# Kernel tuning notes

Measured on AMD Instinct MI355X. Metric: run time of the kernel, lower is better.

The kernel has to match this reference:

```python
import jax, jax.numpy as jnp
import numpy as np


def setup_inputs() -> dict:
    key = jax.random.key(0)
    k1, k2 = jax.random.split(key)
    B, N, M, D = 8, 2048, 2048, 1024
    x = jax.random.normal(k1, (B, N, D), dtype=jnp.float32)
    y = jax.random.normal(k2, (B, M, D), dtype=jnp.float32)
    return {"x": x, "y": y}


def reference(x, y):
    # scores: [B, N, M] = x @ y^T
    scores = jnp.einsum("bnd,bmd->bnm", x, y)
    # row-normalized attention over M (axis=2 of scores)
    attn_row = jax.nn.softmax(scores, axis=2)
    # column-normalized attention: softmax over N of scores^T, i.e. axis=1 then transpose
    attn_col = jax.nn.softmax(scores, axis=1)  # [B, N, M], normalized over N
    A = jnp.einsum("bnm,bmd->bnd", attn_row, y)          # attended summary of y per x-token
    Bout = jnp.einsum("bnm,bnd->bmd", attn_col, x)       # attended summary of x per y-token
    return (A, Bout)
```

## Files before the change

### kernel.cpp

```cpp
#include <hip/hip_runtime.h>
#include <cstdint>
#include <cstddef>

namespace {

constexpr int Bb = 8;
constexpr int Nn = 2048;
constexpr int Dd = 1024;
constexpr int NT = 64;

typedef _Float16 half8 __attribute__((ext_vector_type(8)));
typedef float f32x4v __attribute__((ext_vector_type(4)));
typedef float f32x16v __attribute__((ext_vector_type(16)));
typedef unsigned int v2u __attribute__((ext_vector_type(2)));
typedef unsigned int v4u __attribute__((ext_vector_type(4)));

__device__ __forceinline__ float fast_exp2(float x) {
  float r;
  asm("v_exp_f32 %0, %1\n\ts_nop 1" : "=v"(r) : "v"(x));
  return r;
}

__device__ __forceinline__ unsigned cvt2(float a, float b) {
  return __builtin_bit_cast(unsigned, __builtin_amdgcn_cvt_pkrtz(a, b));
}

__device__ __forceinline__ void barrier_lgkm() {
  asm volatile("s_waitcnt lgkmcnt(0)" ::: "memory");
  __builtin_amdgcn_s_barrier();
  __builtin_amdgcn_sched_barrier(0);
}
__device__ __forceinline__ void barrier_plain() {
  __builtin_amdgcn_s_barrier();
  __builtin_amdgcn_sched_barrier(0);
}

__global__ void convf16(const float* __restrict__ in, v4u* __restrict__ out) {
  const int n8 = Bb * Nn * Dd / 8;
  int i = blockIdx.x * blockDim.x + threadIdx.x;
  const int stride = gridDim.x * blockDim.x;
  const f32x4v* in4 = (const f32x4v*)in;
  for (; i < n8; i += stride) {
    f32x4v a = in4[2 * i], b = in4[2 * i + 1];
    v4u p;
    p[0] = cvt2(a[0], a[1]);
    p[1] = cvt2(a[2], a[3]);
    p[2] = cvt2(b[0], b[1]);
    p[3] = cvt2(b[2], b[3]);
    out[i] = p;
  }
}

template <int WS>
__device__ __forceinline__ v4u ld8h(const float* f32p, const v4u* h16p) {
  if constexpr (WS) {
    return *h16p;
  } else {
    f32x4v a = *(const f32x4v*)f32p;
    f32x4v b = *(const f32x4v*)(f32p + 4);
    v4u p;
    p[0] = cvt2(a[0], a[1]);
    p[1] = cvt2(a[2], a[3]);
    p[2] = cvt2(b[0], b[1]);
    p[3] = cvt2(b[2], b[3]);
    return p;
  }
}

template <int WS>
__global__ __launch_bounds__(512, 2) void flash_fwd(
    const float* __restrict__ Qf, const float* __restrict__ Yf,
    const v4u* __restrict__ Qw, const v4u* __restrict__ Yw,
    float* __restrict__ Om) {
  __shared__ __attribute__((aligned(128))) char ybuf[65536];
  __shared__ __attribute__((aligned(16))) char pscr[16384];
  __shared__ __attribute__((aligned(16))) char Pb[2048];
  __shared__ float sscale[32];
  __shared__ float sinvl[32];
  __shared__ int sflag[2];

  const int tid = (int)threadIdx.x;
  const int w = tid >> 6, l = tid & 63;
  const int lm = l & 15, g = (l >> 4) & 3, g2 = (l >> 5) & 1, l31 = l & 31;
  const int kvf = w >> 2, ds = w & 3;
  const int bid = (int)blockIdx.x, batch = bid & 7, row0 = (bid >> 3) * 32;
  const size_t bY = (size_t)batch * Nn;

  v4u qreg[2][8];
#pragma unroll
  for (int qh = 0; qh < 2; ++qh)
#pragma unroll
    for (int ks = 0; ks < 8; ++ks) {
      const int rr = row0 + qh * 16 + lm;
      const int dd_ = ds * 256 + ks * 32 + g * 8;
      qreg[qh][ks] = ld8h<WS>(Qf + (size_t)(bY + rr) * Dd + dd_,
                              Qw + (size_t)(bY + rr) * 128 + (dd_ >> 3));
    }

#define LOADY(dst, t_)                                                        \
  do {                                                                        \
    const int rr_ = (t_)*32 + kvf * 16 + lm;                                  \
    _Pragma("unroll") for (int ks = 0; ks < 8; ++ks) {                        \
      const int dd_ = ds * 256 + ks * 32 + g * 8;                             \
      dst[ks] = ld8h<WS>(Yf + (size_t)(bY + rr_) * Dd + dd_,                  \
                         Yw + (size_t)(bY + rr_) * 128 + (dd_ >> 3));         \
    }                                                                         \
  } while (0)

  const unsigned sbase =
      (unsigned)((kvf * 4 + (lm >> 2)) * 8192 + (ds * 16 + (g >> 1)) * 128 +
                 (lm & 3) * 32 + (g & 1) * 16);
#define STAGE_WR(SRC)                                                         \
  do {                                                                        \
    _Pragma("unroll") for (int ks = 0; ks < 8; ++ks)                          \
        *(v4u*)(ybuf + sbase + ks * 256) = SRC[ks];                           \
  } while (0)

  v4u sA[8], sB[8];
  LOADY(sA, 0);
  STAGE_WR(sA);

  f32x16v Oacc[4];
#pragma unroll
  for (int i = 0; i < 4; ++i)
#pragma unroll
    for (int j = 0; j < 16; ++j) Oacc[i][j] = 0.0f;

  float m_run = -__builtin_inff();
  float l_run = 0.0f;
  const unsigned ylds = (unsigned)(uintptr_t)&ybuf[0];
  constexpr float L2E = 1.44269504088896f;

  __syncthreads();

#define TILE_BODY(CUR, NXT, t_)                                               \
  do {                                                                        \
    f32x4v acc0 = {0.f, 0.f, 0.f, 0.f}, acc1 = {0.f, 0.f, 0.f, 0.f};          \
    _Pragma("unroll") for (int ks = 0; ks < 8; ++ks) {                        \
      half8 av = __builtin_bit_cast(half8, CUR[ks]);                          \
      acc0 = __builtin_amdgcn_mfma_f32_16x16x32_f16(                          \
          av, __builtin_bit_cast(half8, qreg[0][ks]), acc0, 0, 0, 0);         \
      acc1 = __builtin_amdgcn_mfma_f32_16x16x32_f16(                          \
          av, __builtin_bit_cast(half8, qreg[1][ks]), acc1, 0, 0, 0);         \
    }                                                                         \
    LOADY(NXT, ((t_) + 1) & 63);                                              \
    *(f32x4v*)(pscr + (w * 2 + 0) * 1024 + l * 16) = acc0;                    \
    *(f32x4v*)(pscr + (w * 2 + 1) * 1024 + l * 16) = acc1;                    \
    barrier_lgkm();                       \
    if (w < 2) {                                                              \
      const int qh = w;                                                       \
      f32x4v sa = {0.f, 0.f, 0.f, 0.f}, sb = {0.f, 0.f, 0.f, 0.f};            \
      _Pragma("unroll") for (int s = 0; s < 4; ++s) {                         \
        sa += *(const f32x4v*)(pscr + (s * 2 + qh) * 1024 + l * 16);          \
        sb += *(const f32x4v*)(pscr + ((s + 4) * 2 + qh) * 1024 + l * 16);    \
      }                                                                       \
      float pm = fmaxf(fmaxf(fmaxf(sa[0], sa[1]), fmaxf(sa[2], sa[3])),       \
                       fmaxf(fmaxf(sb[0], sb[1]), fmaxf(sb[2], sb[3])));      \
      pm = fmaxf(pm, __shfl_xor(pm, 16));                                     \
      pm = fmaxf(pm, __shfl_xor(pm, 32));                                     \
      bool defer = (pm <= m_run + 8.0f);                                      \
      bool allw = (bool)__all((int)defer);                                    \
      float scale = 1.0f;                                                     \
      if (!allw) {                                                            \
        float mn = fmaxf(m_run, pm);                                          \
        scale = fast_exp2((m_run - mn) * L2E);                                \
        m_run = mn;                                                           \
      }                                                                       \
      f32x4v ea, eb;                                                          \
      _Pragma("unroll") for (int i = 0; i < 4; ++i) {                         \
        ea[i] = fast_exp2((sa[i] - m_run) * L2E);                             \
        eb[i] = fast_exp2((sb[i] - m_run) * L2E);                             \
      }                                                                       \
      float ps = (ea[0] + ea[1]) + (ea[2] + ea[3]) + (eb[0] + eb[1]) +        \
                 (eb[2] + eb[3]);                                             \
      ps += __shfl_xor(ps, 16);                                               \
      ps += __shfl_xor(ps, 32);                                               \
      l_run = l_run * scale + ps;                                             \
      const int q_ = qh * 16 + lm;                                            \
      v2u pw0, pw1;                                                           \
      pw0[0] = cvt2(ea[0], ea[1]);                                            \
      pw0[1] = cvt2(ea[2], ea[3]);                                            \
      pw1[0] = cvt2(eb[0], eb[1]);                                            \
      pw1[1] = cvt2(eb[2], eb[3]);                                            \
      *(v2u*)(Pb + (g >> 1) * 512 + q_ * 16 + (g & 1) * 8) = pw0;             \
      *(v2u*)(Pb + (2 + (g >> 1)) * 512 + q_ * 16 + (g & 1) * 8) = pw1;       \
      if (l < 16) sscale[q_] = scale;                                         \
      if (l == 0) sflag[qh] = allw ? 0 : 1;                                   \
    }                                                                         \
    barrier_lgkm();                                \
    if (sflag[0] | sflag[1]) {                                                \
      _Pragma("unroll") for (int df = 0; df < 4; ++df)                        \
          _Pragma("unroll") for (int r = 0; r < 16; ++r) {                    \
        const int q_ = (r & 3) + 8 * (r >> 2) + 4 * g2;                       \
        Oacc[df][r] *= sscale[q_];                                            \
      }                                                                       \
    }                                                                         \
    _Pragma("unroll") for (int kb = 0; kb < 2; ++kb) {                        \
      half8 pa = *(const half8*)(Pb + (kb * 2 + g2) * 512 + l31 * 16);        \
      v2u trr[8];                                                             \
      _Pragma("unroll") for (int df = 0; df < 4; ++df) {                      \
        const unsigned wb =                                                   \
            ylds + (unsigned)((kb * 4 + g2 * 2) * 8192 +                      \
                              ((w * 4 + df) * 2 + (l31 >> 4)) * 128 +         \
                              (l31 & 15) * 8);                                \
        asm volatile("ds_read_b64_tr_b16 %0, %1"                              \
                     : "=v"(trr[df * 2])                                      \
                     : "v"(wb));                                              \
        asm volatile("ds_read_b64_tr_b16 %0, %1"                              \
                     : "=v"(trr[df * 2 + 1])                                  \
                     : "v"(wb + 8192u));                                      \
      }                                                                       \
    asm volatile("s_waitcnt lgkmcnt(0)" ::: "memory");                        \
    __builtin_amdgcn_sched_barrier(0);                                        \
      _Pragma("unroll") for (int df = 0; df < 4; ++df) {                      \
        v4u bu;                                                               \
        bu[0] = trr[df * 2][0];                                               \
        bu[1] = trr[df * 2][1];                                               \
        bu[2] = trr[df * 2 + 1][0];                                           \
        bu[3] = trr[df * 2 + 1][1];                                           \
        Oacc[df] = __builtin_amdgcn_mfma_f32_32x32x16_f16(                    \
            pa, __builtin_bit_cast(half8, bu), Oacc[df], 0, 0, 0);            \
      }                                                                       \
    }                                                                         \
    barrier_plain();                        \
    STAGE_WR(NXT);                                                            \
  } while (0)

  for (int t = 0; t < NT; t += 2) {
    TILE_BODY(sA, sB, t);
    TILE_BODY(sB, sA, t + 1);
  }

  if (w < 2 && l < 16) sinvl[w * 16 + lm] = 1.0f / l_run;
  __syncthreads();
#pragma unroll
  for (int df = 0; df < 4; ++df)
#pragma unroll
    for (int r = 0; r < 16; ++r) {
      const int q_ = (r & 3) + 8 * (r >> 2) + 4 * g2;
      const float inv = sinvl[q_];
      Om[(size_t)(bY + row0 + q_) * Dd + (w * 4 + df) * 32 + l31] =
          Oacc[df][r] * inv;
    }
#undef TILE_BODY
#undef STAGE_WR
#undef LOADY
}

}

extern "C" void kernel_launch(void* const* d_in, const int* in_sizes, int n_in,
                              void* d_out, int out_size, void* d_ws,
                              size_t ws_size, hipStream_t stream) {
  (void)in_sizes; (void)n_in; (void)out_size;
  const float* x = (const float*)d_in[0];
  const float* y = (const float*)d_in[1];
  float* A = (float*)d_out;
  float* Bo = A + (size_t)Bb * Nn * Dd;
  const size_t halfws = (size_t)Bb * Nn * Dd * 2;
  dim3 fg(512), fb(512);
  if (d_ws != nullptr && ws_size >= 2 * halfws) {
    v4u* Xw = (v4u*)d_ws;
    v4u* Yw = (v4u*)((char*)d_ws + halfws);
    hipLaunchKernelGGL(convf16, dim3(2048), dim3(256), 0, stream, x, Xw);
    hipLaunchKernelGGL(convf16, dim3(2048), dim3(256), 0, stream, y, Yw);
    hipLaunchKernelGGL(flash_fwd<1>, fg, fb, 0, stream, x, y, Xw, Yw, A);
    hipLaunchKernelGGL(flash_fwd<1>, fg, fb, 0, stream, y, x, Yw, Xw, Bo);
  } else {
    hipLaunchKernelGGL(flash_fwd<0>, fg, fb, 0, stream, x, y, (const v4u*)x,
                       (const v4u*)y, A);
    hipLaunchKernelGGL(flash_fwd<0>, fg, fb, 0, stream, y, x, (const v4u*)y,
                       (const v4u*)x, Bo);
  }
}
```

Measured before the change: 590.6 us.

## Software-pipeline PV matmul of previous tile with QK scores of current tile

Restructures the flash-attention-style loop so the P·V MFMA work for tile t-1 is issued (LDS transposed reads of Y and P) before, and finished after, the QK score MFMAs of tile t. The global load of the next Y tile moves to the start of the body, and the staged LDS write now happens after the softmax step, dropping one barrier per tile. This targets latency of LDS reads and barrier stalls, at the cost of more live registers (16 trr regs plus two P fragments) and an epilogue PV step.

```diff
diff --git a/kernel.cpp b/kernel.cpp
--- a/kernel.cpp
+++ b/kernel.cpp
@@ -27,10 +27,6 @@
 
 __device__ __forceinline__ void barrier_lgkm() {
   asm volatile("s_waitcnt lgkmcnt(0)" ::: "memory");
-  __builtin_amdgcn_s_barrier();
-  __builtin_amdgcn_sched_barrier(0);
-}
-__device__ __forceinline__ void barrier_plain() {
   __builtin_amdgcn_s_barrier();
   __builtin_amdgcn_sched_barrier(0);
 }
@@ -118,7 +114,6 @@
 
   v4u sA[8], sB[8];
   LOADY(sA, 0);
-  STAGE_WR(sA);
 
   f32x16v Oacc[4];
 #pragma unroll
@@ -131,10 +126,55 @@
   const unsigned ylds = (unsigned)(uintptr_t)&ybuf[0];
   constexpr float L2E = 1.44269504088896f;
 
-  __syncthreads();
-
-#define TILE_BODY(CUR, NXT, t_)                                               \
-  do {                                                                        \
+  half8 pa0, pa1;
+  v2u trr[16];
+
+#define PV_ISSUE()                                                            \
+  do {                                                                        \
+    pa0 = *(const half8*)(Pb + g2 * 512 + l31 * 16);                          \
+    pa1 = *(const half8*)(Pb + (2 + g2) * 512 + l31 * 16);                    \
+    _Pragma("unroll") for (int kb = 0; kb < 2; ++kb)                          \
+        _Pragma("unroll") for (int df = 0; df < 4; ++df) {                    \
+      const unsigned wb =                                                     \
+          ylds + (unsigned)((kb * 4 + g2 * 2) * 8192 +                        \
+                            ((w * 4 + df) * 2 + (l31 >> 4)) * 128 +           \
+                            (l31 & 15) * 8);                                  \
+      asm volatile("ds_read_b64_tr_b16 %0, %1"                                \
+                   : "=v"(trr[kb * 8 + df * 2])                               \
+                   : "v"(wb));                                                \
+      asm volatile("ds_read_b64_tr_b16 %0, %1"                                \
+                   : "=v"(trr[kb * 8 + df * 2 + 1])                           \
+                   : "v"(wb + 8192u));                                        \
+    }                                                                         \
+  } while (0)
+
+#define PV_FINISH()                                                           \
+  do {                                                                        \
+    if (sflag[0] | sflag[1]) {                                                \
+      _Pragma("unroll") for (int df = 0; df < 4; ++df)                        \
+          _Pragma("unroll") for (int r = 0; r < 16; ++r) {                    \
+        const int q_ = (r & 3) + 8 * (r >> 2) + 4 * g2;                       \
+        Oacc[df][r] *= sscale[q_];                                            \
+      }                                                                       \
+    }                                                                         \
+    asm volatile("s_waitcnt lgkmcnt(0)" ::: "memory");                        \
+    __builtin_amdgcn_sched_barrier(0);                                        \
+    _Pragma("unroll") for (int kb = 0; kb < 2; ++kb)                          \
+        _Pragma("unroll") for (int df = 0; df < 4; ++df) {                    \
+      v4u bu;                                                                 \
+      bu[0] = trr[kb * 8 + df * 2][0];                                        \
+      bu[1] = trr[kb * 8 + df * 2][1];                                        \
+      bu[2] = trr[kb * 8 + df * 2 + 1][0];                                    \
+      bu[3] = trr[kb * 8 + df * 2 + 1][1];                                    \
+      Oacc[df] = __builtin_amdgcn_mfma_f32_32x32x16_f16(                      \
+          kb ? pa1 : pa0, __builtin_bit_cast(half8, bu), Oacc[df], 0, 0, 0);  \
+    }                                                                         \
+  } while (0)
+
+#define TILE_BODY(CUR, NXT, t_, DOPV)                                         \
+  do {                                                                        \
+    LOADY(NXT, ((t_) + 1) & 63);                                              \
+    if (DOPV) PV_ISSUE();                                                     \
     f32x4v acc0 = {0.f, 0.f, 0.f, 0.f}, acc1 = {0.f, 0.f, 0.f, 0.f};          \
     _Pragma("unroll") for (int ks = 0; ks < 8; ++ks) {                        \
       half8 av = __builtin_bit_cast(half8, CUR[ks]);                          \
@@ -143,10 +183,10 @@
       acc1 = __builtin_amdgcn_mfma_f32_16x16x32_f16(                          \
           av, __builtin_bit_cast(half8, qreg[1][ks]), acc1, 0, 0, 0);         \
     }                                                                         \
-    LOADY(NXT, ((t_) + 1) & 63);                                              \
     *(f32x4v*)(pscr + (w * 2 + 0) * 1024 + l * 16) = acc0;                    \
     *(f32x4v*)(pscr + (w * 2 + 1) * 1024 + l * 16) = acc1;                    \
-    barrier_lgkm();                       \
+    if (DOPV) PV_FINISH();                                                    \
+    barrier_lgkm();               \
     if (w < 2) {                                                              \
       const int qh = w;                                                       \
       f32x4v sa = {0.f, 0.f, 0.f, 0.f}, sb = {0.f, 0.f, 0.f, 0.f};            \
@@ -187,49 +227,18 @@
       if (l < 16) sscale[q_] = scale;                                         \
       if (l == 0) sflag[qh] = allw ? 0 : 1;                                   \
     }                                                                         \
-    barrier_lgkm();                                \
-    if (sflag[0] | sflag[1]) {                                                \
-      _Pragma("unroll") for (int df = 0; df < 4; ++df)                        \
-          _Pragma("unroll") for (int r = 0; r < 16; ++r) {                    \
-        const int q_ = (r & 3) + 8 * (r >> 2) + 4 * g2;                       \
-        Oacc[df][r] *= sscale[q_];                                            \
-      }                                                                       \
-    }                                                                         \
-    _Pragma("unroll") for (int kb = 0; kb < 2; ++kb) {                        \
-      half8 pa = *(const half8*)(Pb + (kb * 2 + g2) * 512 + l31 * 16);        \
-      v2u trr[8];                                                             \
-      _Pragma("unroll") for (int df = 0; df < 4; ++df) {                      \
-        const unsigned wb =                                                   \
-            ylds + (unsigned)((kb * 4 + g2 * 2) * 8192 +                      \
-                              ((w * 4 + df) * 2 + (l31 >> 4)) * 128 +         \
-                              (l31 & 15) * 8);                                \
-        asm volatile("ds_read_b64_tr_b16 %0, %1"                              \
-                     : "=v"(trr[df * 2])                                      \
-                     : "v"(wb));                                              \
-        asm volatile("ds_read_b64_tr_b16 %0, %1"                              \
-                     : "=v"(trr[df * 2 + 1])                                  \
-                     : "v"(wb + 8192u));                                      \
-      }                                                                       \
-    asm volatile("s_waitcnt lgkmcnt(0)" ::: "memory");                        \
-    __builtin_amdgcn_sched_barrier(0);                                        \
-      _Pragma("unroll") for (int df = 0; df < 4; ++df) {                      \
-        v4u bu;                                                               \
-        bu[0] = trr[df * 2][0];                                               \
-        bu[1] = trr[df * 2][1];                                               \
-        bu[2] = trr[df * 2 + 1][0];                                           \
-        bu[3] = trr[df * 2 + 1][1];                                           \
-        Oacc[df] = __builtin_amdgcn_mfma_f32_32x32x16_f16(                    \
-            pa, __builtin_bit_cast(half8, bu), Oacc[df], 0, 0, 0);            \
-      }                                                                       \
-    }                                                                         \
-    barrier_plain();                        \
-    STAGE_WR(NXT);                                                            \
-  } while (0)
-
-  for (int t = 0; t < NT; t += 2) {
-    TILE_BODY(sA, sB, t);
-    TILE_BODY(sB, sA, t + 1);
-  }
+    STAGE_WR(CUR);                                                            \
+    barrier_lgkm();                    \
+  } while (0)
+
+  TILE_BODY(sA, sB, 0, 0);
+  TILE_BODY(sB, sA, 1, 1);
+  for (int t = 2; t < NT; t += 2) {
+    TILE_BODY(sA, sB, t, 1);
+    TILE_BODY(sB, sA, t + 1, 1);
+  }
+  PV_ISSUE();
+  PV_FINISH();
 
   if (w < 2 && l < 16) sinvl[w * 16 + lm] = 1.0f / l_run;
   __syncthreads();
@@ -243,6 +252,8 @@
           Oacc[df][r] * inv;
     }
 #undef TILE_BODY
+#undef PV_FINISH
+#undef PV_ISSUE
 #undef STAGE_WR
 #undef LOADY
 }
```

Result: slower. 1.087 ms (+84.1%).

## Double-buffer Y tile in LDS and spread softmax across all waves

Applied to the files above, without the earlier changes.

The Y tile staging buffer is now double-buffered, so the next tile is written to LDS right after this tile's transposed reads are issued, and one barrier per iteration is removed. The softmax reduction is spread over all 8 waves, each handling 4 query rows with DPP row reductions, instead of being done by 2 waves while the other 6 sit idle. The rescale flag is double-buffered to avoid a race. In exchange, LDS use roughly doubles (about 150KB), which may limit the launch bound of 2 blocks per CU, and register pressure rises because 16 trr registers are held.

```diff
diff --git a/kernel.cpp b/kernel.cpp
--- a/kernel.cpp
+++ b/kernel.cpp
@@ -10,6 +10,7 @@
 constexpr int NT = 64;
 
 typedef _Float16 half8 __attribute__((ext_vector_type(8)));
+typedef float f32x2v __attribute__((ext_vector_type(2)));
 typedef float f32x4v __attribute__((ext_vector_type(4)));
 typedef float f32x16v __attribute__((ext_vector_type(16)));
 typedef unsigned int v2u __attribute__((ext_vector_type(2)));
@@ -25,12 +26,34 @@
   return __builtin_bit_cast(unsigned, __builtin_amdgcn_cvt_pkrtz(a, b));
 }
 
+template <int CTRL>
+__device__ __forceinline__ float dpp_f(float v) {
+  return __builtin_bit_cast(
+      float, __builtin_amdgcn_update_dpp(0, __builtin_bit_cast(int, v), CTRL,
+                                         0xF, 0xF, true));
+}
+__device__ __forceinline__ float red16_max(float v) {
+  v = fmaxf(v, dpp_f<0xB1>(v));
+  v = fmaxf(v, dpp_f<0x4E>(v));
+  v = fmaxf(v, dpp_f<0x124>(v));
+  v = fmaxf(v, dpp_f<0x128>(v));
+  return v;
+}
+__device__ __forceinline__ float red16_add(float v) {
+  v = v + dpp_f<0xB1>(v);
+  v = v + dpp_f<0x4E>(v);
+  v = v + dpp_f<0x124>(v);
+  v = v + dpp_f<0x128>(v);
+  return v;
+}
+
 __device__ __forceinline__ void barrier_lgkm() {
   asm volatile("s_waitcnt lgkmcnt(0)" ::: "memory");
   __builtin_amdgcn_s_barrier();
   __builtin_amdgcn_sched_barrier(0);
 }
-__device__ __forceinline__ void barrier_plain() {
+__device__ __forceinline__ void barrier_lgkm15() {
+  asm volatile("s_waitcnt lgkmcnt(15)" ::: "memory");
   __builtin_amdgcn_s_barrier();
   __builtin_amdgcn_sched_barrier(0);
 }
@@ -72,12 +95,12 @@
     const float* __restrict__ Qf, const float* __restrict__ Yf,
     const v4u* __restrict__ Qw, const v4u* __restrict__ Yw,
     float* __restrict__ Om) {
-  __shared__ __attribute__((aligned(128))) char ybuf[65536];
-  __shared__ __attribute__((aligned(16))) char pscr[16384];
+  __shared__ __attribute__((aligned(128))) char ybuf[2][65536];
+  __shared__ __attribute__((aligned(16))) float pscr2[4][32][36];
   __shared__ __attribute__((aligned(16))) char Pb[2048];
   __shared__ float sscale[32];
   __shared__ float sinvl[32];
-  __shared__ int sflag[2];
+  __shared__ int flags[2];
 
   const int tid = (int)threadIdx.x;
   const int w = tid >> 6, l = tid & 63;
@@ -110,15 +133,20 @@
   const unsigned sbase =
       (unsigned)((kvf * 4 + (lm >> 2)) * 8192 + (ds * 16 + (g >> 1)) * 128 +
                  (lm & 3) * 32 + (g & 1) * 16);
-#define STAGE_WR(SRC)                                                         \
+#define STAGE_WR(SRC, BASE)                                                   \
   do {                                                                        \
     _Pragma("unroll") for (int ks = 0; ks < 8; ++ks)                          \
-        *(v4u*)(ybuf + sbase + ks * 256) = SRC[ks];                           \
+        *(v4u*)((BASE) + sbase + ks * 256) = SRC[ks];                         \
   } while (0)
 
-  v4u sA[8], sB[8];
-  LOADY(sA, 0);
-  STAGE_WR(sA);
+  char* const yb0 = &ybuf[0][0];
+  v4u s[8];
+  LOADY(s, 0);
+  STAGE_WR(s, yb0);
+  if (tid == 0) {
+    flags[0] = 0;
+    flags[1] = 0;
+  }
 
   f32x16v Oacc[4];
 #pragma unroll
@@ -128,110 +156,106 @@
 
   float m_run = -__builtin_inff();
   float l_run = 0.0f;
-  const unsigned ylds = (unsigned)(uintptr_t)&ybuf[0];
+  const unsigned ylds = (unsigned)(uintptr_t)yb0;
   constexpr float L2E = 1.44269504088896f;
 
   __syncthreads();
 
-#define TILE_BODY(CUR, NXT, t_)                                               \
-  do {                                                                        \
-    f32x4v acc0 = {0.f, 0.f, 0.f, 0.f}, acc1 = {0.f, 0.f, 0.f, 0.f};          \
-    _Pragma("unroll") for (int ks = 0; ks < 8; ++ks) {                        \
-      half8 av = __builtin_bit_cast(half8, CUR[ks]);                          \
-      acc0 = __builtin_amdgcn_mfma_f32_16x16x32_f16(                          \
-          av, __builtin_bit_cast(half8, qreg[0][ks]), acc0, 0, 0, 0);         \
-      acc1 = __builtin_amdgcn_mfma_f32_16x16x32_f16(                          \
-          av, __builtin_bit_cast(half8, qreg[1][ks]), acc1, 0, 0, 0);         \
-    }                                                                         \
-    LOADY(NXT, ((t_) + 1) & 63);                                              \
-    *(f32x4v*)(pscr + (w * 2 + 0) * 1024 + l * 16) = acc0;                    \
-    *(f32x4v*)(pscr + (w * 2 + 1) * 1024 + l * 16) = acc1;                    \
-    barrier_lgkm();                       \
-    if (w < 2) {                                                              \
-      const int qh = w;                                                       \
-      f32x4v sa = {0.f, 0.f, 0.f, 0.f}, sb = {0.f, 0.f, 0.f, 0.f};            \
-      _Pragma("unroll") for (int s = 0; s < 4; ++s) {                         \
-        sa += *(const f32x4v*)(pscr + (s * 2 + qh) * 1024 + l * 16);          \
-        sb += *(const f32x4v*)(pscr + ((s + 4) * 2 + qh) * 1024 + l * 16);    \
-      }                                                                       \
-      float pm = fmaxf(fmaxf(fmaxf(sa[0], sa[1]), fmaxf(sa[2], sa[3])),       \
-                       fmaxf(fmaxf(sb[0], sb[1]), fmaxf(sb[2], sb[3])));      \
-      pm = fmaxf(pm, __shfl_xor(pm, 16));                                     \
-      pm = fmaxf(pm, __shfl_xor(pm, 32));                                     \
-      bool defer = (pm <= m_run + 8.0f);                                      \
-      bool allw = (bool)__all((int)defer);                                    \
-      float scale = 1.0f;                                                     \
-      if (!allw) {                                                            \
-        float mn = fmaxf(m_run, pm);                                          \
-        scale = fast_exp2((m_run - mn) * L2E);                                \
-        m_run = mn;                                                           \
-      }                                                                       \
-      f32x4v ea, eb;                                                          \
-      _Pragma("unroll") for (int i = 0; i < 4; ++i) {                         \
-        ea[i] = fast_exp2((sa[i] - m_run) * L2E);                             \
-        eb[i] = fast_exp2((sb[i] - m_run) * L2E);                             \
-      }                                                                       \
-      float ps = (ea[0] + ea[1]) + (ea[2] + ea[3]) + (eb[0] + eb[1]) +        \
-                 (eb[2] + eb[3]);                                             \
-      ps += __shfl_xor(ps, 16);                                               \
-      ps += __shfl_xor(ps, 32);                                               \
-      l_run = l_run * scale + ps;                                             \
-      const int q_ = qh * 16 + lm;                                            \
-      v2u pw0, pw1;                                                           \
-      pw0[0] = cvt2(ea[0], ea[1]);                                            \
-      pw0[1] = cvt2(ea[2], ea[3]);                                            \
-      pw1[0] = cvt2(eb[0], eb[1]);                                            \
-      pw1[1] = cvt2(eb[2], eb[3]);                                            \
-      *(v2u*)(Pb + (g >> 1) * 512 + q_ * 16 + (g & 1) * 8) = pw0;             \
-      *(v2u*)(Pb + (2 + (g >> 1)) * 512 + q_ * 16 + (g & 1) * 8) = pw1;       \
-      if (l < 16) sscale[q_] = scale;                                         \
-      if (l == 0) sflag[qh] = allw ? 0 : 1;                                   \
-    }                                                                         \
-    barrier_lgkm();                                \
-    if (sflag[0] | sflag[1]) {                                                \
-      _Pragma("unroll") for (int df = 0; df < 4; ++df)                        \
-          _Pragma("unroll") for (int r = 0; r < 16; ++r) {                    \
-        const int q_ = (r & 3) + 8 * (r >> 2) + 4 * g2;                       \
-        Oacc[df][r] *= sscale[q_];                                            \
-      }                                                                       \
-    }                                                                         \
-    _Pragma("unroll") for (int kb = 0; kb < 2; ++kb) {                        \
-      half8 pa = *(const half8*)(Pb + (kb * 2 + g2) * 512 + l31 * 16);        \
-      v2u trr[8];                                                             \
-      _Pragma("unroll") for (int df = 0; df < 4; ++df) {                      \
-        const unsigned wb =                                                   \
-            ylds + (unsigned)((kb * 4 + g2 * 2) * 8192 +                      \
-                              ((w * 4 + df) * 2 + (l31 >> 4)) * 128 +         \
-                              (l31 & 15) * 8);                                \
-        asm volatile("ds_read_b64_tr_b16 %0, %1"                              \
-                     : "=v"(trr[df * 2])                                      \
-                     : "v"(wb));                                              \
-        asm volatile("ds_read_b64_tr_b16 %0, %1"                              \
-                     : "=v"(trr[df * 2 + 1])                                  \
-                     : "v"(wb + 8192u));                                      \
-      }                                                                       \
-    asm volatile("s_waitcnt lgkmcnt(0)" ::: "memory");                        \
-    __builtin_amdgcn_sched_barrier(0);                                        \
-      _Pragma("unroll") for (int df = 0; df < 4; ++df) {                      \
-        v4u bu;                                                               \
-        bu[0] = trr[df * 2][0];                                               \
-        bu[1] = trr[df * 2][1];                                               \
-        bu[2] = trr[df * 2 + 1][0];                                           \
-        bu[3] = trr[df * 2 + 1][1];                                           \
-        Oacc[df] = __builtin_amdgcn_mfma_f32_32x32x16_f16(                    \
-            pa, __builtin_bit_cast(half8, bu), Oacc[df], 0, 0, 0);            \
-      }                                                                       \
-    }                                                                         \
-    barrier_plain();                        \
-    STAGE_WR(NXT);                                                            \
-  } while (0)
-
-  for (int t = 0; t < NT; t += 2) {
-    TILE_BODY(sA, sB, t);
-    TILE_BODY(sB, sA, t + 1);
-  }
-
-  if (w < 2 && l < 16) sinvl[w * 16 + lm] = 1.0f / l_run;
+  for (int t = 0; t < NT; ++t) {
+    const unsigned ytr = ylds + (unsigned)((t & 1) * 65536);
+    char* const ybn = yb0 + (((t + 1) & 1) * 65536);
+
+    f32x4v acc0 = {0.f, 0.f, 0.f, 0.f}, acc1 = {0.f, 0.f, 0.f, 0.f};
+#pragma unroll
+    for (int ks = 0; ks < 8; ++ks) {
+      half8 av = __builtin_bit_cast(half8, s[ks]);
+      acc0 = __builtin_amdgcn_mfma_f32_16x16x32_f16(
+          av, __builtin_bit_cast(half8, qreg[0][ks]), acc0, 0, 0, 0);
+      acc1 = __builtin_amdgcn_mfma_f32_16x16x32_f16(
+          av, __builtin_bit_cast(half8, qreg[1][ks]), acc1, 0, 0, 0);
+    }
+    LOADY(s, (t + 1) & 63);
+    *(f32x4v*)&pscr2[ds][lm][kvf * 16 + g * 4] = acc0;
+    *(f32x4v*)&pscr2[ds][16 + lm][kvf * 16 + g * 4] = acc1;
+    barrier_lgkm();
+
+    {
+      const int rq = 4 * w + (l >> 4);
+      const int c = l & 15;
+      float s0 = 0.f, s1 = 0.f;
+#pragma unroll
+      for (int sl = 0; sl < 4; ++sl) {
+        f32x2v p_ = *(const f32x2v*)&pscr2[sl][rq][2 * c];
+        s0 += p_[0];
+        s1 += p_[1];
+      }
+      float pm = red16_max(fmaxf(s0, s1));
+      bool defer = (pm <= m_run + 8.0f);
+      bool allw = (bool)__all((int)defer);
+      float scale = 1.0f;
+      if (!allw) {
+        float mn = fmaxf(m_run, pm);
+        scale = fast_exp2((m_run - mn) * L2E);
+        m_run = mn;
+      }
+      float e0 = fast_exp2((s0 - m_run) * L2E);
+      float e1 = fast_exp2((s1 - m_run) * L2E);
+      float ps = red16_add(e0 + e1);
+      l_run = l_run * scale + ps;
+      *(unsigned*)(Pb + (c >> 2) * 512 + rq * 16 + (c & 3) * 4) = cvt2(e0, e1);
+      if (c == 0) sscale[rq] = scale;
+      if (l == 0 && !allw) flags[t & 1] = 1;
+    }
+    if (tid == 0) flags[(t + 1) & 1] = 0;
+
+    v2u trr[16];
+#pragma unroll
+    for (int kb = 0; kb < 2; ++kb)
+#pragma unroll
+      for (int df = 0; df < 4; ++df) {
+        const unsigned wb =
+            ytr + (unsigned)((kb * 4 + g2 * 2) * 8192 +
+                             ((w * 4 + df) * 2 + (l31 >> 4)) * 128 +
+                             (l31 & 15) * 8);
+        asm volatile("ds_read_b64_tr_b16 %0, %1"
+                     : "=v"(trr[kb * 8 + df * 2])
+                     : "v"(wb));
+        asm volatile("ds_read_b64_tr_b16 %0, %1"
+                     : "=v"(trr[kb * 8 + df * 2 + 1])
+                     : "v"(wb + 8192u));
+      }
+    STAGE_WR(s, ybn);
+    barrier_lgkm15();
+
+    const int flg = flags[t & 1];
+    half8 pa0 = *(const half8*)(Pb + g2 * 512 + l31 * 16);
+    half8 pa1 = *(const half8*)(Pb + (2 + g2) * 512 + l31 * 16);
+    if (flg) {
+#pragma unroll
+      for (int df = 0; df < 4; ++df)
+#pragma unroll
+        for (int r = 0; r < 16; ++r) {
+          const int q_ = (r & 3) + 8 * (r >> 2) + 4 * g2;
+          Oacc[df][r] *= sscale[q_];
+        }
+    }
+    asm volatile("s_waitcnt lgkmcnt(0)" ::: "memory");
+    __builtin_amdgcn_sched_barrier(0);
+#pragma unroll
+    for (int kb = 0; kb < 2; ++kb)
+#pragma unroll
+      for (int df = 0; df < 4; ++df) {
+        v4u bu;
+        bu[0] = trr[kb * 8 + df * 2][0];
+        bu[1] = trr[kb * 8 + df * 2][1];
+        bu[2] = trr[kb * 8 + df * 2 + 1][0];
+        bu[3] = trr[kb * 8 + df * 2 + 1][1];
+        Oacc[df] = __builtin_amdgcn_mfma_f32_32x32x16_f16(
+            kb ? pa1 : pa0, __builtin_bit_cast(half8, bu), Oacc[df], 0, 0, 0);
+      }
+  }
+
+  if ((l & 15) == 0) sinvl[4 * w + (l >> 4)] = 1.0f / l_run;
   __syncthreads();
 #pragma unroll
   for (int df = 0; df < 4; ++df)
@@ -242,7 +266,6 @@
       Om[(size_t)(bY + row0 + q_) * Dd + (w * 4 + df) * 32 + l31] =
           Oacc[df][r] * inv;
     }
-#undef TILE_BODY
 #undef STAGE_WR
 #undef LOADY
 }
```

New measurement: 661.1 us. +11.9%, slower.
